# Performance work log

Hardware: AMD Instinct MI355X
Metric: run time of the kernel (lower is better)

## Reference

```python
import jax, jax.numpy as jnp
import numpy as np

EPS = 1e-6


def setup_inputs() -> dict:
    key = jax.random.key(0)
    k1, k2, k3 = jax.random.split(key, 3)
    N, E, CIN, COUT = 50000, 800000, 128, 128
    x = jax.random.normal(k1, (N, CIN), dtype=jnp.float32)
    edge_index = jax.random.randint(k2, (2, E), 0, N, dtype=jnp.int64)
    # Xavier-uniform weight as in reset_parameters
    limit = float(np.sqrt(6.0 / (CIN + COUT)))
    weight = jax.random.uniform(k3, (CIN, COUT), minval=-limit, maxval=limit, dtype=jnp.float32)
    bias = jnp.zeros((COUT,), dtype=jnp.float32)
    return {"x": x, "edge_index": edge_index, "weight": weight, "bias": bias}


def reference(x, edge_index, weight, bias):
    # x: [N, Cin], edge_index: [2, E]
    N = x.shape[0]
    src, dst = edge_index[0], edge_index[1]
    ones = jnp.ones(src.shape, dtype=x.dtype)
    # degree counts (== torch.bincount with minlength=N)
    src_deg = jax.ops.segment_sum(ones, src, num_segments=N)  # [N]
    dst_deg = jax.ops.segment_sum(ones, dst, num_segments=N)  # [N]
    src_inv = jax.lax.rsqrt(src_deg + EPS)
    dst_inv = jax.lax.rsqrt(dst_deg + EPS)
    edge_norm = src_inv[src] * dst_inv[dst]  # [E]
    msg = x[src] * edge_norm[:, None]  # [E, Cin] normalized source features
    # Equivalent to the dense one-hot einsum('ef,en->nf'): segment-sum over dst
    aggregated = jax.ops.segment_sum(msg, dst, num_segments=N)  # [N, Cin]
    # add_self_loops=False branch
    return aggregated @ weight + bias
```

## Files before the change

### kernel.cpp

```cpp
#include <hip/hip_runtime.h>
#include <math.h>

#define EPS 1e-6f
#define CAP 64
#define RANGES 16
#define SLICES 32
#define HBLK  (RANGES * SLICES)

__device__ inline unsigned short f2bf(float f) {
    unsigned u = __float_as_uint(f);
    unsigned r = u + 0x7FFFu + ((u >> 16) & 1u);
    return (unsigned short)(r >> 16);
}

__global__ __launch_bounds__(256, 2)
void k_fused(const int* __restrict__ ei, int E,
             int* __restrict__ deg_src, int* __restrict__ deg_dst,
             int* __restrict__ slots,
             const float* __restrict__ x, const float* __restrict__ w,
             unsigned short* __restrict__ y, int N, int G) {
    __shared__ float4 wlds[128 * 32];
    int b = (int)blockIdx.x;
    int t = (int)threadIdx.x;

    int role, idx;
    if (b < 3 * HBLK) { role = b % 3; idx = b / 3; }
    else {
        int b2 = b - 3 * HBLK;
        int twoRegion = 2 * (G - HBLK);
        if (b2 < twoRegion) { role = b2 & 1; idx = HBLK + (b2 >> 1); }
        else                { role = 1;      idx = G + (b2 - twoRegion); }
    }

    if (role == 2) {
        int r  = idx / SLICES;
        int sl = idx - r * SLICES;
        int binsPerRange = (N + RANGES - 1) / RANGES;
        int base = r * binsPerRange;
        int hi = N - base; if (hi > binsPerRange) hi = binsPerRange;
        if (hi <= 0) return;
        int* bins = (int*)wlds;
        for (int i = t; i < binsPerRange; i += 256) bins[i] = 0;
        __syncthreads();

        int sliceLen = (E + SLICES - 1) / SLICES;
        int eBeg = sl * sliceLen;
        int eEnd = eBeg + sliceLen; if (eEnd > E) eEnd = E;
        int vBeg = (eBeg + 3) & ~3;
        int vEnd = eEnd & ~3;
        for (int i = eBeg + t; i < (vBeg < eEnd ? vBeg : eEnd); i += 256) {
            int a = ei[i] - base;
            if ((unsigned)a < (unsigned)hi) atomicAdd(&bins[a], 1);
        }
        const int4* e4 = (const int4*)ei;
        int q0 = vBeg >> 2, q1 = vEnd >> 2;
        #pragma unroll 4
        for (int i = q0 + t; i < q1; i += 256) {
            int4 v = e4[i];
            int a;
            a = v.x - base; if ((unsigned)a < (unsigned)hi) atomicAdd(&bins[a], 1);
            a = v.y - base; if ((unsigned)a < (unsigned)hi) atomicAdd(&bins[a], 1);
            a = v.z - base; if ((unsigned)a < (unsigned)hi) atomicAdd(&bins[a], 1);
            a = v.w - base; if ((unsigned)a < (unsigned)hi) atomicAdd(&bins[a], 1);
        }
        for (int i = (vEnd > vBeg ? vEnd : vBeg) + t; i < eEnd; i += 256) {
            int a = ei[i] - base;
            if ((unsigned)a < (unsigned)hi) atomicAdd(&bins[a], 1);
        }
        __syncthreads();
        for (int i = t; i < hi; i += 256) {
            int v = bins[i];
            if (v) atomicAdd(&deg_src[base + i], v);
        }
        return;
    }

    if (role == 1) {
        int e = idx * 256 + t;
        if (e < E) {
            int s = ei[e];
            int d = ei[E + e];
            int r = atomicAdd(&deg_dst[d], 1);
            if (r < CAP) slots[(size_t)d * CAP + r] = s;
        }
        return;
    }

    const float4* w4 = (const float4*)w;
    #pragma unroll
    for (int i = 0; i < 16; ++i)
        wlds[t + 256 * i] = w4[t + 256 * i];
    __syncthreads();

    int tx = t & 31;
    int ty = t >> 5;
    int rowBase = idx * 64 + ty * 8;

    float4 acc[8];
    #pragma unroll
    for (int r = 0; r < 8; ++r) acc[r] = make_float4(0.f, 0.f, 0.f, 0.f);

    const float4* x4 = (const float4*)x;

    if (rowBase + 8 <= N) {
        #pragma unroll 1
        for (int k4 = 0; k4 < 32; ++k4) {
            float4 xv[8];
            #pragma unroll
            for (int r = 0; r < 8; ++r)
                xv[r] = x4[(size_t)(rowBase + r) * 32 + k4];
            #pragma unroll
            for (int kk = 0; kk < 4; ++kk) {
                float4 wv = wlds[(k4 * 4 + kk) * 32 + tx];
                #pragma unroll
                for (int r = 0; r < 8; ++r) {
                    float xs = (kk == 0) ? xv[r].x : (kk == 1) ? xv[r].y
                             : (kk == 2) ? xv[r].z : xv[r].w;
                    acc[r].x += xs * wv.x;
                    acc[r].y += xs * wv.y;
                    acc[r].z += xs * wv.z;
                    acc[r].w += xs * wv.w;
                }
            }
        }
        #pragma unroll
        for (int r = 0; r < 8; ++r) {
            ushort4 us;
            us.x = f2bf(acc[r].x); us.y = f2bf(acc[r].y);
            us.z = f2bf(acc[r].z); us.w = f2bf(acc[r].w);
            ((ushort4*)(y + (size_t)(rowBase + r) * 128))[tx] = us;
        }
    } else {
        #pragma unroll 1
        for (int k4 = 0; k4 < 32; ++k4) {
            float4 xv[8];
            #pragma unroll
            for (int r = 0; r < 8; ++r)
                xv[r] = (rowBase + r < N) ? x4[(size_t)(rowBase + r) * 32 + k4]
                                          : make_float4(0.f, 0.f, 0.f, 0.f);
            #pragma unroll
            for (int kk = 0; kk < 4; ++kk) {
                float4 wv = wlds[(k4 * 4 + kk) * 32 + tx];
                #pragma unroll
                for (int r = 0; r < 8; ++r) {
                    float xs = (kk == 0) ? xv[r].x : (kk == 1) ? xv[r].y
                             : (kk == 2) ? xv[r].z : xv[r].w;
                    acc[r].x += xs * wv.x;
                    acc[r].y += xs * wv.y;
                    acc[r].z += xs * wv.z;
                    acc[r].w += xs * wv.w;
                }
            }
        }
        #pragma unroll
        for (int r = 0; r < 8; ++r) {
            if (rowBase + r < N) {
                ushort4 us;
                us.x = f2bf(acc[r].x); us.y = f2bf(acc[r].y);
                us.z = f2bf(acc[r].z); us.w = f2bf(acc[r].w);
                ((ushort4*)(y + (size_t)(rowBase + r) * 128))[tx] = us;
            }
        }
    }
}

__launch_bounds__(256)
__global__ void k_gather(const int* __restrict__ deg_src, const int* __restrict__ deg_dst,
                         const int* __restrict__ slots,
                         const unsigned* __restrict__ y1,
                         const float* __restrict__ bias,
                         float* __restrict__ out, int N) {
    int gid  = blockIdx.x * blockDim.x + threadIdx.x;
    int node = gid >> 6;
    int lane = gid & 63;
    if (node >= N) return;
    int dd  = deg_dst[node];
    int end = dd < CAP ? dd : CAP;
    const int* list = slots + (size_t)node * CAP;

    float ax0 = 0.f, ay0 = 0.f, ax1 = 0.f, ay1 = 0.f;
    float ax2 = 0.f, ay2 = 0.f, ax3 = 0.f, ay3 = 0.f;

    int j = 0;
    #pragma unroll 1
    for (; j + 16 <= end; j += 16) {
        int s[16]; unsigned v[16]; float c[16];
        #pragma unroll
        for (int u = 0; u < 16; ++u) s[u] = list[j + u];
        #pragma unroll
        for (int u = 0; u < 16; ++u) v[u] = y1[(size_t)s[u] * 64 + lane];
        #pragma unroll
        for (int u = 0; u < 16; ++u) c[u] = rsqrtf((float)deg_src[s[u]] + EPS);
        #pragma unroll
        for (int u = 0; u < 16; u += 4) {
            ax0 += c[u+0] * __uint_as_float(v[u+0] << 16); ay0 += c[u+0] * __uint_as_float(v[u+0] & 0xffff0000u);
            ax1 += c[u+1] * __uint_as_float(v[u+1] << 16); ay1 += c[u+1] * __uint_as_float(v[u+1] & 0xffff0000u);
            ax2 += c[u+2] * __uint_as_float(v[u+2] << 16); ay2 += c[u+2] * __uint_as_float(v[u+2] & 0xffff0000u);
            ax3 += c[u+3] * __uint_as_float(v[u+3] << 16); ay3 += c[u+3] * __uint_as_float(v[u+3] & 0xffff0000u);
        }
    }
    if (j + 8 <= end) {
        int s[8]; unsigned v[8]; float c[8];
        #pragma unroll
        for (int u = 0; u < 8; ++u) s[u] = list[j + u];
        #pragma unroll
        for (int u = 0; u < 8; ++u) v[u] = y1[(size_t)s[u] * 64 + lane];
        #pragma unroll
        for (int u = 0; u < 8; ++u) c[u] = rsqrtf((float)deg_src[s[u]] + EPS);
        #pragma unroll
        for (int u = 0; u < 8; u += 4) {
            ax0 += c[u+0] * __uint_as_float(v[u+0] << 16); ay0 += c[u+0] * __uint_as_float(v[u+0] & 0xffff0000u);
            ax1 += c[u+1] * __uint_as_float(v[u+1] << 16); ay1 += c[u+1] * __uint_as_float(v[u+1] & 0xffff0000u);
            ax2 += c[u+2] * __uint_as_float(v[u+2] << 16); ay2 += c[u+2] * __uint_as_float(v[u+2] & 0xffff0000u);
            ax3 += c[u+3] * __uint_as_float(v[u+3] << 16); ay3 += c[u+3] * __uint_as_float(v[u+3] & 0xffff0000u);
        }
        j += 8;
    }
    if (j + 4 <= end) {
        int s0 = list[j + 0], s1 = list[j + 1];
        int s2 = list[j + 2], s3 = list[j + 3];
        unsigned v0 = y1[(size_t)s0 * 64 + lane];
        unsigned v1 = y1[(size_t)s1 * 64 + lane];
        unsigned v2 = y1[(size_t)s2 * 64 + lane];
        unsigned v3 = y1[(size_t)s3 * 64 + lane];
        float c0 = rsqrtf((float)deg_src[s0] + EPS);
        float c1 = rsqrtf((float)deg_src[s1] + EPS);
        float c2 = rsqrtf((float)deg_src[s2] + EPS);
        float c3 = rsqrtf((float)deg_src[s3] + EPS);
        ax0 += c0 * __uint_as_float(v0 << 16); ay0 += c0 * __uint_as_float(v0 & 0xffff0000u);
        ax1 += c1 * __uint_as_float(v1 << 16); ay1 += c1 * __uint_as_float(v1 & 0xffff0000u);
        ax2 += c2 * __uint_as_float(v2 << 16); ay2 += c2 * __uint_as_float(v2 & 0xffff0000u);
        ax3 += c3 * __uint_as_float(v3 << 16); ay3 += c3 * __uint_as_float(v3 & 0xffff0000u);
        j += 4;
    }
    #pragma unroll 1
    for (; j < end; ++j) {
        int s = list[j];
        unsigned v = y1[(size_t)s * 64 + lane];
        float c = rsqrtf((float)deg_src[s] + EPS);
        ax0 += c * __uint_as_float(v << 16); ay0 += c * __uint_as_float(v & 0xffff0000u);
    }

    float nd = rsqrtf((float)dd + EPS);
    float accx = ((ax0 + ax1) + (ax2 + ax3)) * nd;
    float accy = ((ay0 + ay1) + (ay2 + ay3)) * nd;
    float2 b = ((const float2*)bias)[lane];
    ((float2*)out)[(size_t)node * 64 + lane] = make_float2(accx + b.x, accy + b.y);
}

extern "C" void kernel_launch(void* const* d_in, const int* in_sizes, int n_in,
                              void* d_out, int out_size, void* d_ws, size_t ws_size,
                              hipStream_t stream) {
    const float* x    = (const float*)d_in[0];
    const int*   ei   = (const int*)d_in[1];
    const float* w    = (const float*)d_in[2];
    const float* bias = (const float*)d_in[3];
    float*       out  = (float*)d_out;

    const int C = 128;
    const int N = in_sizes[0] / C;
    const int E = in_sizes[1] / 2;

    char* ws = (char*)d_ws;
    size_t off = 0;
    auto alloc = [&](size_t bytes) -> void* {
        void* p = ws + off;
        off += (bytes + 255) & ~(size_t)255;
        return p;
    };
    int*            degblk = (int*)alloc((size_t)2 * N * 4);
    int*            slots  = (int*)alloc((size_t)N * CAP * 4);
    unsigned short* y      = (unsigned short*)alloc((size_t)N * C * 2);
    (void)ws_size;
    int* deg_src = degblk;
    int* deg_dst = degblk + N;

    const int TB = 256;
    hipMemsetAsync(degblk, 0, (size_t)2 * N * 4, stream);

    int degBlocks  = (E + TB - 1) / TB;
    int gemmBlocks = (N + 63) / 64;
    int grid = HBLK + degBlocks + gemmBlocks;
    k_fused<<<grid, TB, 0, stream>>>(
        ei, E, deg_src, deg_dst, slots, x, w, y, N, gemmBlocks);

    long long gthreads = (long long)N * 64;
    k_gather<<<(int)((gthreads + TB - 1) / TB), TB, 0, stream>>>(
        deg_src, deg_dst, slots, (const unsigned*)y, bias, out, N);
}
```

Measured before the change: 182.8 us.

## Merge all stages into one persistent kernel with a software grid barrier

The fused scatter/GEMM kernel and the gather kernel become one persistent kernel of 512 blocks. Odd blocks split between the GEMM and the source-degree histogram in fixed ratios. All blocks then claim destination-slot work dynamically through an atomic counter, pass a spin-wait grid barrier, and run the gather in a grid-stride loop. This removes the second launch and the idle gap between kernels, and balances the edge scatter across blocks. In exchange it relies on all 512 blocks being resident at once, since otherwise the barrier deadlocks. The fixed role split may also leave the GEMM or the histogram as a straggler that holds up the barrier.

```diff
diff --git a/kernel.cpp b/kernel.cpp
--- a/kernel.cpp
+++ b/kernel.cpp
@@ -6,6 +6,11 @@
 #define RANGES 16
 #define SLICES 32
 #define HBLK  (RANGES * SLICES)
+#define NBLK  512
+#define TB    256
+#define GEMB  192
+#define HSTB  64
+#define SCHUNK 4
 
 __device__ inline unsigned short f2bf(float f) {
     unsigned u = __float_as_uint(f);
@@ -13,239 +18,270 @@
     return (unsigned short)(r >> 16);
 }
 
-__global__ __launch_bounds__(256, 2)
-void k_fused(const int* __restrict__ ei, int E,
-             int* __restrict__ deg_src, int* __restrict__ deg_dst,
-             int* __restrict__ slots,
-             const float* __restrict__ x, const float* __restrict__ w,
-             unsigned short* __restrict__ y, int N, int G) {
+__device__ inline void grid_barrier(int* cnt, int* flag) {
+    __syncthreads();
+    if (threadIdx.x == 0) {
+        int a = __hip_atomic_fetch_add(cnt, 1, __ATOMIC_ACQ_REL, __HIP_MEMORY_SCOPE_AGENT);
+        if (a == NBLK - 1) {
+            __hip_atomic_store(flag, 1, __ATOMIC_RELEASE, __HIP_MEMORY_SCOPE_AGENT);
+        } else {
+            while (__hip_atomic_load(flag, __ATOMIC_ACQUIRE, __HIP_MEMORY_SCOPE_AGENT) == 0)
+                __builtin_amdgcn_s_sleep(8);
+        }
+    }
+    __syncthreads();
+}
+
+__global__ __launch_bounds__(TB, 2)
+void k_mega(const int* __restrict__ ei, int E,
+            int* __restrict__ deg_src, int* __restrict__ deg_dst,
+            int* __restrict__ slots,
+            const float* __restrict__ x, const float* __restrict__ w,
+            unsigned short* __restrict__ y,
+            const float* __restrict__ bias, float* __restrict__ out,
+            int N, int G, int* __restrict__ ctl) {
     __shared__ float4 wlds[128 * 32];
+    __shared__ int sbase;
     int b = (int)blockIdx.x;
     int t = (int)threadIdx.x;
 
-    int role, idx;
-    if (b < 3 * HBLK) { role = b % 3; idx = b / 3; }
-    else {
-        int b2 = b - 3 * HBLK;
-        int twoRegion = 2 * (G - HBLK);
-        if (b2 < twoRegion) { role = b2 & 1; idx = HBLK + (b2 >> 1); }
-        else                { role = 1;      idx = G + (b2 - twoRegion); }
-    }
-
-    if (role == 2) {
-        int r  = idx / SLICES;
-        int sl = idx - r * SLICES;
-        int binsPerRange = (N + RANGES - 1) / RANGES;
-        int base = r * binsPerRange;
-        int hi = N - base; if (hi > binsPerRange) hi = binsPerRange;
-        if (hi <= 0) return;
-        int* bins = (int*)wlds;
-        for (int i = t; i < binsPerRange; i += 256) bins[i] = 0;
-        __syncthreads();
-
-        int sliceLen = (E + SLICES - 1) / SLICES;
-        int eBeg = sl * sliceLen;
-        int eEnd = eBeg + sliceLen; if (eEnd > E) eEnd = E;
-        int vBeg = (eBeg + 3) & ~3;
-        int vEnd = eEnd & ~3;
-        for (int i = eBeg + t; i < (vBeg < eEnd ? vBeg : eEnd); i += 256) {
-            int a = ei[i] - base;
-            if ((unsigned)a < (unsigned)hi) atomicAdd(&bins[a], 1);
-        }
-        const int4* e4 = (const int4*)ei;
-        int q0 = vBeg >> 2, q1 = vEnd >> 2;
-        #pragma unroll 4
-        for (int i = q0 + t; i < q1; i += 256) {
-            int4 v = e4[i];
-            int a;
-            a = v.x - base; if ((unsigned)a < (unsigned)hi) atomicAdd(&bins[a], 1);
-            a = v.y - base; if ((unsigned)a < (unsigned)hi) atomicAdd(&bins[a], 1);
-            a = v.z - base; if ((unsigned)a < (unsigned)hi) atomicAdd(&bins[a], 1);
-            a = v.w - base; if ((unsigned)a < (unsigned)hi) atomicAdd(&bins[a], 1);
-        }
-        for (int i = (vEnd > vBeg ? vEnd : vBeg) + t; i < eEnd; i += 256) {
-            int a = ei[i] - base;
-            if ((unsigned)a < (unsigned)hi) atomicAdd(&bins[a], 1);
-        }
-        __syncthreads();
-        for (int i = t; i < hi; i += 256) {
-            int v = bins[i];
-            if (v) atomicAdd(&deg_src[base + i], v);
-        }
-        return;
-    }
-
-    if (role == 1) {
-        int e = idx * 256 + t;
-        if (e < E) {
-            int s = ei[e];
-            int d = ei[E + e];
-            int r = atomicAdd(&deg_dst[d], 1);
-            if (r < CAP) slots[(size_t)d * CAP + r] = s;
-        }
-        return;
-    }
-
-    const float4* w4 = (const float4*)w;
-    #pragma unroll
-    for (int i = 0; i < 16; ++i)
-        wlds[t + 256 * i] = w4[t + 256 * i];
-    __syncthreads();
-
-    int tx = t & 31;
-    int ty = t >> 5;
-    int rowBase = idx * 64 + ty * 8;
-
-    float4 acc[8];
-    #pragma unroll
-    for (int r = 0; r < 8; ++r) acc[r] = make_float4(0.f, 0.f, 0.f, 0.f);
-
-    const float4* x4 = (const float4*)x;
-
-    if (rowBase + 8 <= N) {
-        #pragma unroll 1
-        for (int k4 = 0; k4 < 32; ++k4) {
-            float4 xv[8];
-            #pragma unroll
-            for (int r = 0; r < 8; ++r)
-                xv[r] = x4[(size_t)(rowBase + r) * 32 + k4];
-            #pragma unroll
-            for (int kk = 0; kk < 4; ++kk) {
-                float4 wv = wlds[(k4 * 4 + kk) * 32 + tx];
+    if (b & 1) {
+        int k = b >> 1;
+        int q = k & 3;
+        if (q < 3) {
+            int gi = (k >> 2) * 3 + q;
+            const float4* w4 = (const float4*)w;
+            #pragma unroll
+            for (int i = 0; i < 16; ++i)
+                wlds[t + 256 * i] = w4[t + 256 * i];
+            __syncthreads();
+            int tx = t & 31;
+            int ty = t >> 5;
+            const float4* x4 = (const float4*)x;
+            for (int it = gi; it < G; it += GEMB) {
+                int rowBase = it * 64 + ty * 8;
+                float4 acc[8];
                 #pragma unroll
-                for (int r = 0; r < 8; ++r) {
-                    float xs = (kk == 0) ? xv[r].x : (kk == 1) ? xv[r].y
-                             : (kk == 2) ? xv[r].z : xv[r].w;
-                    acc[r].x += xs * wv.x;
-                    acc[r].y += xs * wv.y;
-                    acc[r].z += xs * wv.z;
-                    acc[r].w += xs * wv.w;
+                for (int r = 0; r < 8; ++r) acc[r] = make_float4(0.f, 0.f, 0.f, 0.f);
+                if (rowBase + 8 <= N) {
+                    #pragma unroll 1
+                    for (int k4 = 0; k4 < 32; ++k4) {
+                        float4 xv[8];
+                        #pragma unroll
+                        for (int r = 0; r < 8; ++r)
+                            xv[r] = x4[(size_t)(rowBase + r) * 32 + k4];
+                        #pragma unroll
+                        for (int kk = 0; kk < 4; ++kk) {
+                            float4 wv = wlds[(k4 * 4 + kk) * 32 + tx];
+                            #pragma unroll
+                            for (int r = 0; r < 8; ++r) {
+                                float xs = (kk == 0) ? xv[r].x : (kk == 1) ? xv[r].y
+                                         : (kk == 2) ? xv[r].z : xv[r].w;
+                                acc[r].x += xs * wv.x;
+                                acc[r].y += xs * wv.y;
+                                acc[r].z += xs * wv.z;
+                                acc[r].w += xs * wv.w;
+                            }
+                        }
+                    }
+                    #pragma unroll
+                    for (int r = 0; r < 8; ++r) {
+                        ushort4 us;
+                        us.x = f2bf(acc[r].x); us.y = f2bf(acc[r].y);
+                        us.z = f2bf(acc[r].z); us.w = f2bf(acc[r].w);
+                        ((ushort4*)(y + (size_t)(rowBase + r) * 128))[tx] = us;
+                    }
+                } else {
+                    #pragma unroll 1
+                    for (int k4 = 0; k4 < 32; ++k4) {
+                        float4 xv[8];
+                        #pragma unroll
+                        for (int r = 0; r < 8; ++r)
+                            xv[r] = (rowBase + r < N) ? x4[(size_t)(rowBase + r) * 32 + k4]
+                                                      : make_float4(0.f, 0.f, 0.f, 0.f);
+                        #pragma unroll
+                        for (int kk = 0; kk < 4; ++kk) {
+                            float4 wv = wlds[(k4 * 4 + kk) * 32 + tx];
+                            #pragma unroll
+                            for (int r = 0; r < 8; ++r) {
+                                float xs = (kk == 0) ? xv[r].x : (kk == 1) ? xv[r].y
+                                         : (kk == 2) ? xv[r].z : xv[r].w;
+                                acc[r].x += xs * wv.x;
+                                acc[r].y += xs * wv.y;
+                                acc[r].z += xs * wv.z;
+                                acc[r].w += xs * wv.w;
+                            }
+                        }
+                    }
+                    #pragma unroll
+                    for (int r = 0; r < 8; ++r) {
+                        if (rowBase + r < N) {
+                            ushort4 us;
+                            us.x = f2bf(acc[r].x); us.y = f2bf(acc[r].y);
+                            us.z = f2bf(acc[r].z); us.w = f2bf(acc[r].w);
+                            ((ushort4*)(y + (size_t)(rowBase + r) * 128))[tx] = us;
+                        }
+                    }
                 }
             }
-        }
-        #pragma unroll
-        for (int r = 0; r < 8; ++r) {
-            ushort4 us;
-            us.x = f2bf(acc[r].x); us.y = f2bf(acc[r].y);
-            us.z = f2bf(acc[r].z); us.w = f2bf(acc[r].w);
-            ((ushort4*)(y + (size_t)(rowBase + r) * 128))[tx] = us;
-        }
-    } else {
-        #pragma unroll 1
-        for (int k4 = 0; k4 < 32; ++k4) {
-            float4 xv[8];
-            #pragma unroll
-            for (int r = 0; r < 8; ++r)
-                xv[r] = (rowBase + r < N) ? x4[(size_t)(rowBase + r) * 32 + k4]
-                                          : make_float4(0.f, 0.f, 0.f, 0.f);
-            #pragma unroll
-            for (int kk = 0; kk < 4; ++kk) {
-                float4 wv = wlds[(k4 * 4 + kk) * 32 + tx];
-                #pragma unroll
-                for (int r = 0; r < 8; ++r) {
-                    float xs = (kk == 0) ? xv[r].x : (kk == 1) ? xv[r].y
-                             : (kk == 2) ? xv[r].z : xv[r].w;
-                    acc[r].x += xs * wv.x;
-                    acc[r].y += xs * wv.y;
-                    acc[r].z += xs * wv.z;
-                    acc[r].w += xs * wv.w;
+        } else {
+            int hidx = k >> 2;
+            int binsPerRange = (N + RANGES - 1) / RANGES;
+            int* bins = (int*)wlds;
+            for (int it = hidx; it < HBLK; it += HSTB) {
+                int rg = it / SLICES;
+                int sl = it - rg * SLICES;
+                int base = rg * binsPerRange;
+                int hi = N - base; if (hi > binsPerRange) hi = binsPerRange;
+                if (hi > 0) {
+                    __syncthreads();
+                    for (int i = t; i < binsPerRange; i += TB) bins[i] = 0;
+                    __syncthreads();
+                    int sliceLen = (E + SLICES - 1) / SLICES;
+                    int eBeg = sl * sliceLen;
+                    int eEnd = eBeg + sliceLen; if (eEnd > E) eEnd = E;
+                    int vBeg = (eBeg + 3) & ~3;
+                    int vEnd = eEnd & ~3;
+                    for (int i = eBeg + t; i < (vBeg < eEnd ? vBeg : eEnd); i += TB) {
+                        int a = ei[i] - base;
+                        if ((unsigned)a < (unsigned)hi) atomicAdd(&bins[a], 1);
+                    }
+                    const int4* e4 = (const int4*)ei;
+                    int q0 = vBeg >> 2, q1 = vEnd >> 2;
+                    #pragma unroll 4
+                    for (int i = q0 + t; i < q1; i += TB) {
+                        int4 v = e4[i];
+                        int a;
+                        a = v.x - base; if ((unsigned)a < (unsigned)hi) atomicAdd(&bins[a], 1);
+                        a = v.y - base; if ((unsigned)a < (unsigned)hi) atomicAdd(&bins[a], 1);
+                        a = v.z - base; if ((unsigned)a < (unsigned)hi) atomicAdd(&bins[a], 1);
+                        a = v.w - base; if ((unsigned)a < (unsigned)hi) atomicAdd(&bins[a], 1);
+                    }
+                    for (int i = (vEnd > vBeg ? vEnd : vBeg) + t; i < eEnd; i += TB) {
+                        int a = ei[i] - base;
+                        if ((unsigned)a < (unsigned)hi) atomicAdd(&bins[a], 1);
+                    }
+                    __syncthreads();
+                    for (int i = t; i < hi; i += TB) {
+                        int v = bins[i];
+                        if (v) atomicAdd(&deg_src[base + i], v);
+                    }
                 }
             }
         }
-        #pragma unroll
-        for (int r = 0; r < 8; ++r) {
-            if (rowBase + r < N) {
-                ushort4 us;
-                us.x = f2bf(acc[r].x); us.y = f2bf(acc[r].y);
-                us.z = f2bf(acc[r].z); us.w = f2bf(acc[r].w);
-                ((ushort4*)(y + (size_t)(rowBase + r) * 128))[tx] = us;
+    }
+
+    {
+        const int nItems = (E + TB - 1) / TB;
+        for (;;) {
+            __syncthreads();
+            if (t == 0) sbase = atomicAdd(&ctl[0], SCHUNK);
+            __syncthreads();
+            int base = sbase;
+            if (base >= nItems) break;
+            int e0 = (base + 0) * TB + t;
+            int e1 = (base + 1) * TB + t;
+            int e2 = (base + 2) * TB + t;
+            int e3 = (base + 3) * TB + t;
+            bool p0 = e0 < E, p1 = e1 < E, p2 = e2 < E, p3 = e3 < E;
+            int s0 = 0, s1 = 0, s2 = 0, s3 = 0, d0 = 0, d1 = 0, d2 = 0, d3 = 0;
+            if (p0) { s0 = ei[e0]; d0 = ei[E + e0]; }
+            if (p1) { s1 = ei[e1]; d1 = ei[E + e1]; }
+            if (p2) { s2 = ei[e2]; d2 = ei[E + e2]; }
+            if (p3) { s3 = ei[e3]; d3 = ei[E + e3]; }
+            int r0 = p0 ? atomicAdd(&deg_dst[d0], 1) : CAP;
+            int r1 = p1 ? atomicAdd(&deg_dst[d1], 1) : CAP;
+            int r2 = p2 ? atomicAdd(&deg_dst[d2], 1) : CAP;
+            int r3 = p3 ? atomicAdd(&deg_dst[d3], 1) : CAP;
+            if (r0 < CAP) slots[(size_t)d0 * CAP + r0] = s0;
+            if (r1 < CAP) slots[(size_t)d1 * CAP + r1] = s1;
+            if (r2 < CAP) slots[(size_t)d2 * CAP + r2] = s2;
+            if (r3 < CAP) slots[(size_t)d3 * CAP + r3] = s3;
+        }
+    }
+
+    grid_barrier(&ctl[1], &ctl[2]);
+
+    const unsigned* y1 = (const unsigned*)y;
+    int wv   = t >> 6;
+    int lane = t & 63;
+    int nGroups = (N + 3) >> 2;
+    for (int g = b; g < nGroups; g += NBLK) {
+        int node = g * 4 + wv;
+        if (node >= N) continue;
+        int dd  = deg_dst[node];
+        int end = dd < CAP ? dd : CAP;
+        const int* list = slots + (size_t)node * CAP;
+
+        float ax0 = 0.f, ay0 = 0.f, ax1 = 0.f, ay1 = 0.f;
+        float ax2 = 0.f, ay2 = 0.f, ax3 = 0.f, ay3 = 0.f;
+
+        int j = 0;
+        #pragma unroll 1
+        for (; j + 16 <= end; j += 16) {
+            int s[16]; unsigned v[16]; float c[16];
+            #pragma unroll
+            for (int u = 0; u < 16; ++u) s[u] = list[j + u];
+            #pragma unroll
+            for (int u = 0; u < 16; ++u) v[u] = y1[(size_t)s[u] * 64 + lane];
+            #pragma unroll
+            for (int u = 0; u < 16; ++u) c[u] = rsqrtf((float)deg_src[s[u]] + EPS);
+            #pragma unroll
+            for (int u = 0; u < 16; u += 4) {
+                ax0 += c[u+0] * __uint_as_float(v[u+0] << 16); ay0 += c[u+0] * __uint_as_float(v[u+0] & 0xffff0000u);
+                ax1 += c[u+1] * __uint_as_float(v[u+1] << 16); ay1 += c[u+1] * __uint_as_float(v[u+1] & 0xffff0000u);
+                ax2 += c[u+2] * __uint_as_float(v[u+2] << 16); ay2 += c[u+2] * __uint_as_float(v[u+2] & 0xffff0000u);
+                ax3 += c[u+3] * __uint_as_float(v[u+3] << 16); ay3 += c[u+3] * __uint_as_float(v[u+3] & 0xffff0000u);
             }
         }
+        if (j + 8 <= end) {
+            int s[8]; unsigned v[8]; float c[8];
+            #pragma unroll
+            for (int u = 0; u < 8; ++u) s[u] = list[j + u];
+            #pragma unroll
+            for (int u = 0; u < 8; ++u) v[u] = y1[(size_t)s[u] * 64 + lane];
+            #pragma unroll
+            for (int u = 0; u < 8; ++u) c[u] = rsqrtf((float)deg_src[s[u]] + EPS);
+            #pragma unroll
+            for (int u = 0; u < 8; u += 4) {
+                ax0 += c[u+0] * __uint_as_float(v[u+0] << 16); ay0 += c[u+0] * __uint_as_float(v[u+0] & 0xffff0000u);
+                ax1 += c[u+1] * __uint_as_float(v[u+1] << 16); ay1 += c[u+1] * __uint_as_float(v[u+1] & 0xffff0000u);
+                ax2 += c[u+2] * __uint_as_float(v[u+2] << 16); ay2 += c[u+2] * __uint_as_float(v[u+2] & 0xffff0000u);
+                ax3 += c[u+3] * __uint_as_float(v[u+3] << 16); ay3 += c[u+3] * __uint_as_float(v[u+3] & 0xffff0000u);
+            }
+            j += 8;
+        }
+        if (j + 4 <= end) {
+            int s0 = list[j + 0], s1 = list[j + 1];
+            int s2 = list[j + 2], s3 = list[j + 3];
+            unsigned v0 = y1[(size_t)s0 * 64 + lane];
+            unsigned v1 = y1[(size_t)s1 * 64 + lane];
+            unsigned v2 = y1[(size_t)s2 * 64 + lane];
+            unsigned v3 = y1[(size_t)s3 * 64 + lane];
+            float c0 = rsqrtf((float)deg_src[s0] + EPS);
+            float c1 = rsqrtf((float)deg_src[s1] + EPS);
+            float c2 = rsqrtf((float)deg_src[s2] + EPS);
+            float c3 = rsqrtf((float)deg_src[s3] + EPS);
+            ax0 += c0 * __uint_as_float(v0 << 16); ay0 += c0 * __uint_as_float(v0 & 0xffff0000u);
+            ax1 += c1 * __uint_as_float(v1 << 16); ay1 += c1 * __uint_as_float(v1 & 0xffff0000u);
+            ax2 += c2 * __uint_as_float(v2 << 16); ay2 += c2 * __uint_as_float(v2 & 0xffff0000u);
+            ax3 += c3 * __uint_as_float(v3 << 16); ay3 += c3 * __uint_as_float(v3 & 0xffff0000u);
+            j += 4;
+        }
+        #pragma unroll 1
+        for (; j < end; ++j) {
+            int s = list[j];
+            unsigned v = y1[(size_t)s * 64 + lane];
+            float c = rsqrtf((float)deg_src[s] + EPS);
+            ax0 += c * __uint_as_float(v << 16); ay0 += c * __uint_as_float(v & 0xffff0000u);
+        }
+
+        float nd = rsqrtf((float)dd + EPS);
+        float accx = ((ax0 + ax1) + (ax2 + ax3)) * nd;
+        float accy = ((ay0 + ay1) + (ay2 + ay3)) * nd;
+        float2 bb = ((const float2*)bias)[lane];
+        ((float2*)out)[(size_t)node * 64 + lane] = make_float2(accx + bb.x, accy + bb.y);
     }
-}
-
-__launch_bounds__(256)
-__global__ void k_gather(const int* __restrict__ deg_src, const int* __restrict__ deg_dst,
-                         const int* __restrict__ slots,
-                         const unsigned* __restrict__ y1,
-                         const float* __restrict__ bias,
-                         float* __restrict__ out, int N) {
-    int gid  = blockIdx.x * blockDim.x + threadIdx.x;
-    int node = gid >> 6;
-    int lane = gid & 63;
-    if (node >= N) return;
-    int dd  = deg_dst[node];
-    int end = dd < CAP ? dd : CAP;
-    const int* list = slots + (size_t)node * CAP;
-
-    float ax0 = 0.f, ay0 = 0.f, ax1 = 0.f, ay1 = 0.f;
-    float ax2 = 0.f, ay2 = 0.f, ax3 = 0.f, ay3 = 0.f;
-
-    int j = 0;
-    #pragma unroll 1
-    for (; j + 16 <= end; j += 16) {
-        int s[16]; unsigned v[16]; float c[16];
-        #pragma unroll
-        for (int u = 0; u < 16; ++u) s[u] = list[j + u];
-        #pragma unroll
-        for (int u = 0; u < 16; ++u) v[u] = y1[(size_t)s[u] * 64 + lane];
-        #pragma unroll
-        for (int u = 0; u < 16; ++u) c[u] = rsqrtf((float)deg_src[s[u]] + EPS);
-        #pragma unroll
-        for (int u = 0; u < 16; u += 4) {
-            ax0 += c[u+0] * __uint_as_float(v[u+0] << 16); ay0 += c[u+0] * __uint_as_float(v[u+0] & 0xffff0000u);
-            ax1 += c[u+1] * __uint_as_float(v[u+1] << 16); ay1 += c[u+1] * __uint_as_float(v[u+1] & 0xffff0000u);
-            ax2 += c[u+2] * __uint_as_float(v[u+2] << 16); ay2 += c[u+2] * __uint_as_float(v[u+2] & 0xffff0000u);
-            ax3 += c[u+3] * __uint_as_float(v[u+3] << 16); ay3 += c[u+3] * __uint_as_float(v[u+3] & 0xffff0000u);
-        }
-    }
-    if (j + 8 <= end) {
-        int s[8]; unsigned v[8]; float c[8];
-        #pragma unroll
-        for (int u = 0; u < 8; ++u) s[u] = list[j + u];
-        #pragma unroll
-        for (int u = 0; u < 8; ++u) v[u] = y1[(size_t)s[u] * 64 + lane];
-        #pragma unroll
-        for (int u = 0; u < 8; ++u) c[u] = rsqrtf((float)deg_src[s[u]] + EPS);
-        #pragma unroll
-        for (int u = 0; u < 8; u += 4) {
-            ax0 += c[u+0] * __uint_as_float(v[u+0] << 16); ay0 += c[u+0] * __uint_as_float(v[u+0] & 0xffff0000u);
-            ax1 += c[u+1] * __uint_as_float(v[u+1] << 16); ay1 += c[u+1] * __uint_as_float(v[u+1] & 0xffff0000u);
-            ax2 += c[u+2] * __uint_as_float(v[u+2] << 16); ay2 += c[u+2] * __uint_as_float(v[u+2] & 0xffff0000u);
-            ax3 += c[u+3] * __uint_as_float(v[u+3] << 16); ay3 += c[u+3] * __uint_as_float(v[u+3] & 0xffff0000u);
-        }
-        j += 8;
-    }
-    if (j + 4 <= end) {
-        int s0 = list[j + 0], s1 = list[j + 1];
-        int s2 = list[j + 2], s3 = list[j + 3];
-        unsigned v0 = y1[(size_t)s0 * 64 + lane];
-        unsigned v1 = y1[(size_t)s1 * 64 + lane];
-        unsigned v2 = y1[(size_t)s2 * 64 + lane];
-        unsigned v3 = y1[(size_t)s3 * 64 + lane];
-        float c0 = rsqrtf((float)deg_src[s0] + EPS);
-        float c1 = rsqrtf((float)deg_src[s1] + EPS);
-        float c2 = rsqrtf((float)deg_src[s2] + EPS);
-        float c3 = rsqrtf((float)deg_src[s3] + EPS);
-        ax0 += c0 * __uint_as_float(v0 << 16); ay0 += c0 * __uint_as_float(v0 & 0xffff0000u);
-        ax1 += c1 * __uint_as_float(v1 << 16); ay1 += c1 * __uint_as_float(v1 & 0xffff0000u);
-        ax2 += c2 * __uint_as_float(v2 << 16); ay2 += c2 * __uint_as_float(v2 & 0xffff0000u);
-        ax3 += c3 * __uint_as_float(v3 << 16); ay3 += c3 * __uint_as_float(v3 & 0xffff0000u);
-        j += 4;
-    }
-    #pragma unroll 1
-    for (; j < end; ++j) {
-        int s = list[j];
-        unsigned v = y1[(size_t)s * 64 + lane];
-        float c = rsqrtf((float)deg_src[s] + EPS);
-        ax0 += c * __uint_as_float(v << 16); ay0 += c * __uint_as_float(v & 0xffff0000u);
-    }
-
-    float nd = rsqrtf((float)dd + EPS);
-    float accx = ((ax0 + ax1) + (ax2 + ax3)) * nd;
-    float accy = ((ay0 + ay1) + (ay2 + ay3)) * nd;
-    float2 b = ((const float2*)bias)[lane];
-    ((float2*)out)[(size_t)node * 64 + lane] = make_float2(accx + b.x, accy + b.y);
 }
 
 extern "C" void kernel_launch(void* const* d_in, const int* in_sizes, int n_in,
@@ -268,23 +304,18 @@
         off += (bytes + 255) & ~(size_t)255;
         return p;
     };
+    int*            ctl    = (int*)alloc(256);
     int*            degblk = (int*)alloc((size_t)2 * N * 4);
+    size_t zeroBytes = off;
     int*            slots  = (int*)alloc((size_t)N * CAP * 4);
     unsigned short* y      = (unsigned short*)alloc((size_t)N * C * 2);
     (void)ws_size;
     int* deg_src = degblk;
     int* deg_dst = degblk + N;
 
-    const int TB = 256;
-    hipMemsetAsync(degblk, 0, (size_t)2 * N * 4, stream);
-
-    int degBlocks  = (E + TB - 1) / TB;
+    hipMemsetAsync(ws, 0, zeroBytes, stream);
+
     int gemmBlocks = (N + 63) / 64;
-    int grid = HBLK + degBlocks + gemmBlocks;
-    k_fused<<<grid, TB, 0, stream>>>(
-        ei, E, deg_src, deg_dst, slots, x, w, y, N, gemmBlocks);
-
-    long long gthreads = (long long)N * 64;
-    k_gather<<<(int)((gthreads + TB - 1) / TB), TB, 0, stream>>>(
-        deg_src, deg_dst, slots, (const unsigned*)y, bias, out, N);
+    k_mega<<<NBLK, TB, 0, stream>>>(
+        ei, E, deg_src, deg_dst, slots, x, w, y, bias, out, N, gemmBlocks, ctl);
 }
```

Measured after the change: 361.5 us. 1.98x slower.
